# Kernel optimization log

Hardware: AMD Instinct MI355X
Metric: run time of the kernel (lower is better)

Reference implementation:

```python
import jax, jax.numpy as jnp
import numpy as np

LN_EPS = 1e-5
NORM_EPS = 1e-6
ALPHA = 0.5

def _normalize_xyz_with_pc(pc, xyz):
    # center by point-cloud centroid, scale by max radius (per batch)
    c = pc.mean(axis=1, keepdims=True)                      # [B,1,3]
    scale = jnp.linalg.norm(pc - c, axis=-1).max(axis=1)    # [B]
    return (xyz - c) / (scale[:, None, None] + NORM_EPS)

def setup_inputs() -> dict:
    key = jax.random.key(0)
    ks = jax.random.split(key, 9)
    B, N, Ns, K, Dv, Dc = 4, 20000, 1024, 8192, 768, 256
    return {
        "point_cloud": jax.random.normal(ks[0], (B, N, 3), jnp.float32),
        "seed_xyz": jax.random.normal(ks[1], (B, Ns, 3), jnp.float32),
        "pts": jax.random.normal(ks[2], (B, K, 3), jnp.float32),
        "feat": jax.random.normal(ks[3], (B, Dv, K), jnp.float32),
        "f_graspnet": jax.random.normal(ks[4], (B, Dc, Ns), jnp.float32),
        "W_proj": jax.random.normal(ks[5], (Dc, Dv), jnp.float32) * 0.02,
        "b_proj": jnp.zeros((Dc,), jnp.float32),
        "W_a1": jax.random.normal(ks[6], (Dc, Dc), jnp.float32) * 0.05,
        "b_a1": jnp.zeros((Dc,), jnp.float32),
        "W_a2": jax.random.normal(ks[7], (Dc, Dc), jnp.float32) * 0.05,
        "b_a2": jnp.zeros((Dc,), jnp.float32),
    }

def reference(point_cloud, seed_xyz, pts, feat, f_graspnet,
              W_proj, b_proj, W_a1, b_a1, W_a2, b_a2):
    seed_n = _normalize_xyz_with_pc(point_cloud, seed_xyz)   # [B,Ns,3]
    pts_n = _normalize_xyz_with_pc(point_cloud, pts)         # [B,K,3]
    # squared pairwise distances [B,Ns,K] (argmin equivalent to cdist argmin)
    d2 = ((seed_n ** 2).sum(-1)[:, :, None]
          - 2.0 * jnp.einsum('bnd,bkd->bnk', seed_n, pts_n)
          + (pts_n ** 2).sum(-1)[:, None, :])
    idx = jnp.argmin(d2, axis=-1)                            # [B,Ns]
    vggt_raw = jnp.take_along_axis(feat, idx[:, None, :], axis=2)  # [B,768,Ns]
    # 1x1 conv projector 768->256
    x = jnp.einsum('oc,bcn->bon', W_proj, vggt_raw) + b_proj[None, :, None]
    # LayerNorm over channel dim, no affine
    mu = x.mean(axis=1, keepdims=True)
    var = ((x - mu) ** 2).mean(axis=1, keepdims=True)
    x_ln = (x - mu) / jnp.sqrt(var + LN_EPS)
    # adapter: conv-relu-conv (all 1x1)
    h = jax.nn.relu(jnp.einsum('oc,bcn->bon', W_a1, x_ln) + b_a1[None, :, None])
    f_adapt = jnp.einsum('oc,bcn->bon', W_a2, h) + b_a2[None, :, None]
    return (1.0 - ALPHA) * f_graspnet + ALPHA * f_adapt
```

## Files before the change

kernel.cpp:

```cpp
#include <hip/hip_runtime.h>
#include <hip/hip_bf16.h>
#include <math.h>

#define LN_EPS 1e-5f

constexpr int BB  = 4;
constexpr int NS  = 1024;
constexpr int KP  = 8192;
constexpr int DV  = 768;
constexpr int DC  = 256;

using bf16x8 = __attribute__((ext_vector_type(8))) short;
using f32x4  = __attribute__((ext_vector_type(4))) float;

static __device__ __forceinline__ unsigned short f2bf(float v) {
    __hip_bfloat16 h = __float2bfloat16(v);
    return *reinterpret_cast<unsigned short*>(&h);
}

__global__ __launch_bounds__(256) void argmin_prep_kernel(
    const float* __restrict__ seed_xyz, const float* __restrict__ pts,
    int* __restrict__ out_idx,
    const float* __restrict__ Wp, const float* __restrict__ W1,
    const float* __restrict__ W2,
    unsigned short* __restrict__ Wpb, unsigned short* __restrict__ W1b,
    unsigned short* __restrict__ W2b)
{
    const int t = threadIdx.x;
    if (blockIdx.x >= 512) {
        int e  = (blockIdx.x - 512) * 256 + t;
        int e4 = e << 2;
        const float* src; unsigned short* dst; int off;
        if (e4 < DC * DV)              { src = Wp; dst = Wpb; off = e4; }
        else if (e4 < DC * (DV + DC))  { src = W1; dst = W1b; off = e4 - DC * DV; }
        else                           { src = W2; dst = W2b; off = e4 - DC * (DV + DC); }
        float4 v = *(const float4*)(src + off);
        ushort4 o;
        o.x = f2bf(v.x); o.y = f2bf(v.y); o.z = f2bf(v.z); o.w = f2bf(v.w);
        *(ushort4*)(dst + off) = o;
        return;
    }

    __shared__ float shX[1024], shY[1024], shZ[1024];
    __shared__ double rb[4][8];
    __shared__ int    ri[4][8];

    const int bid  = blockIdx.x;
    const int b    = bid >> 7;
    const int tile = bid & 127;

    double n2sx[8], n2sy[8], n2sz[8];
    {
        const float* sp = seed_xyz + ((size_t)b * NS + tile * 8) * 3;
        #pragma unroll
        for (int ss = 0; ss < 8; ++ss) {
            n2sx[ss] = -2.0 * (double)sp[ss * 3 + 0];
            n2sy[ss] = -2.0 * (double)sp[ss * 3 + 1];
            n2sz[ss] = -2.0 * (double)sp[ss * 3 + 2];
        }
    }

    const float* pb = pts + (size_t)b * KP * 3;
    double best[8];
    int    bidx[8];
    #pragma unroll
    for (int ss = 0; ss < 8; ++ss) { best[ss] = 1e300; bidx[ss] = 0; }

    for (int kt = 0; kt < KP; kt += 1024) {
        #pragma unroll
        for (int q = 0; q < 4; ++q) {
            int i = t + q * 256;
            const float* pp = pb + (size_t)(kt + i) * 3;
            shX[i] = pp[0]; shY[i] = pp[1]; shZ[i] = pp[2];
        }
        __syncthreads();
        #pragma unroll 2
        for (int q = 0; q < 4; ++q) {
            int kl = t + (q << 8);
            double px = (double)shX[kl];
            double py = (double)shY[kl];
            double pz = (double)shZ[kl];
            double h  = fma(px, px, fma(py, py, pz * pz));
            #pragma unroll
            for (int ss = 0; ss < 8; ++ss) {
                double acc = fma(n2sx[ss], px, h);
                acc = fma(n2sy[ss], py, acc);
                acc = fma(n2sz[ss], pz, acc);
                if (acc < best[ss]) { best[ss] = acc; bidx[ss] = kt + kl; }
            }
        }
        __syncthreads();
    }

    #pragma unroll
    for (int o = 1; o < 64; o <<= 1) {
        #pragma unroll
        for (int ss = 0; ss < 8; ++ss) {
            double ob = __shfl_xor(best[ss], o);
            int    oi = __shfl_xor(bidx[ss], o);
            if (ob < best[ss] || (ob == best[ss] && oi < bidx[ss])) {
                best[ss] = ob; bidx[ss] = oi;
            }
        }
    }
    const int w = t >> 6, l = t & 63;
    if (l == 0) {
        #pragma unroll
        for (int ss = 0; ss < 8; ++ss) { rb[w][ss] = best[ss]; ri[w][ss] = bidx[ss]; }
    }
    __syncthreads();
    if (t < 8) {
        double bb = rb[0][t]; int bi = ri[0][t];
        #pragma unroll
        for (int ww = 1; ww < 4; ++ww) {
            double ob = rb[ww][t]; int oi = ri[ww][t];
            if (ob < bb || (ob == bb && oi < bi)) { bb = ob; bi = oi; }
        }
        out_idx[b * NS + tile * 8 + t] = bi;
    }
}

__global__ __launch_bounds__(512) void sort_kernel(
    const int* __restrict__ idx, int* __restrict__ ord, int* __restrict__ ks)
{
    __shared__ int h[512], sc[512], base[512], cnt[512];
    const int b = blockIdx.x;
    const int t = threadIdx.x;
    h[t] = 0; cnt[t] = 0;
    __syncthreads();
    const int k0 = idx[b * NS + t];
    const int k1 = idx[b * NS + 512 + t];
    atomicAdd(&h[k0 >> 4], 1);
    atomicAdd(&h[k1 >> 4], 1);
    __syncthreads();
    sc[t] = h[t];
    __syncthreads();
    #pragma unroll
    for (int st = 1; st < 512; st <<= 1) {
        int add = (t >= st) ? sc[t - st] : 0;
        __syncthreads();
        sc[t] += add;
        __syncthreads();
    }
    base[t] = sc[t] - h[t];
    __syncthreads();
    {
        int bk = k0 >> 4;
        int p  = base[bk] + atomicAdd(&cnt[bk], 1);
        ord[b * NS + p] = t;
        ks [b * NS + p] = k0;
    }
    {
        int bk = k1 >> 4;
        int p  = base[bk] + atomicAdd(&cnt[bk], 1);
        ord[b * NS + p] = 512 + t;
        ks [b * NS + p] = k1;
    }
}

__global__ __launch_bounds__(256) void gather_kernel(
    const float* __restrict__ feat, const int* __restrict__ ord,
    const int* __restrict__ ks, unsigned short* __restrict__ Gb)
{
    const int bid = blockIdx.x;
    const int b   = bid >> 6;
    const int cg  = bid & 63;
    const int c0  = cg * 12;
    const int t   = threadIdx.x;
    const float* fb = feat + ((size_t)b * DV + c0) * KP;

    int sA[4], kA[4];
    #pragma unroll
    for (int i = 0; i < 4; ++i) {
        sA[i] = ord[b * NS + t + i * 256];
        kA[i] = ks [b * NS + t + i * 256];
    }
    float v[4][12];
    #pragma unroll
    for (int i = 0; i < 4; ++i)
        #pragma unroll
        for (int c = 0; c < 12; ++c)
            v[i][c] = fb[(size_t)c * KP + kA[i]];

    #pragma unroll
    for (int i = 0; i < 4; ++i) {
        ushort4 o0, o1, o2;
        o0.x = f2bf(v[i][0]);  o0.y = f2bf(v[i][1]);
        o0.z = f2bf(v[i][2]);  o0.w = f2bf(v[i][3]);
        o1.x = f2bf(v[i][4]);  o1.y = f2bf(v[i][5]);
        o1.z = f2bf(v[i][6]);  o1.w = f2bf(v[i][7]);
        o2.x = f2bf(v[i][8]);  o2.y = f2bf(v[i][9]);
        o2.z = f2bf(v[i][10]); o2.w = f2bf(v[i][11]);
        unsigned short* g = Gb + ((size_t)b * NS + sA[i]) * DV + c0;
        *(ushort4*)(g)     = o0;
        *(ushort4*)(g + 4) = o1;
        *(ushort4*)(g + 8) = o2;
    }
}

__global__ __launch_bounds__(512) void mega_kernel(
    const unsigned short* __restrict__ Gb,
    const float* __restrict__ fg,
    const unsigned short* __restrict__ Wpb, const float* __restrict__ bp,
    const unsigned short* __restrict__ W1b, const float* __restrict__ b1,
    const unsigned short* __restrict__ W2b, const float* __restrict__ b2,
    float* __restrict__ out)
{
    __shared__ alignas(16) unsigned short GtT[16][776];
    __shared__ alignas(16) unsigned short XT[16][264];
    __shared__ alignas(16) unsigned short HT[16][264];
    __shared__ float LNs[8][16];
    __shared__ float LNq[8][16];

    const int bid  = blockIdx.x;
    const int b    = bid >> 6;
    const int tile = bid & 63;
    const int n0   = tile * 16;
    const int t    = threadIdx.x;
    const int w    = t >> 6;
    const int l    = t & 63;
    const int col  = l & 15;
    const int kq   = l >> 4;

    for (int i = t; i < 1536; i += 512) {
        int row = i / 96, c8 = (i % 96) * 8;
        *(bf16x8*)&GtT[row][c8] =
            *(const bf16x8*)&Gb[((size_t)b * NS + n0 + row) * DV + c8];
    }
    __syncthreads();

    f32x4 acc0 = {0.f, 0.f, 0.f, 0.f};
    f32x4 acc1 = {0.f, 0.f, 0.f, 0.f};
    {
        const unsigned short* A0 = Wpb + (size_t)(w * 32 + col) * DV;
        const unsigned short* A1 = Wpb + (size_t)(w * 32 + 16 + col) * DV;
        #pragma unroll 4
        for (int ks = 0; ks < 24; ++ks) {
            int kb = ks * 32 + kq * 8;
            bf16x8 bf = *(const bf16x8*)&GtT[col][kb];
            bf16x8 a0 = *(const bf16x8*)&A0[kb];
            bf16x8 a1 = *(const bf16x8*)&A1[kb];
            acc0 = __builtin_amdgcn_mfma_f32_16x16x32_bf16(a0, bf, acc0, 0, 0, 0);
            acc1 = __builtin_amdgcn_mfma_f32_16x16x32_bf16(a1, bf, acc1, 0, 0, 0);
        }
    }

    float vals[8];
    float s = 0.f, q = 0.f;
    #pragma unroll
    for (int r = 0; r < 4; ++r) {
        int ch0 = w * 32 + kq * 4 + r;
        float v0 = acc0[r] + bp[ch0];
        float v1 = acc1[r] + bp[ch0 + 16];
        vals[r]     = v0;
        vals[4 + r] = v1;
        s += v0 + v1;
        q += v0 * v0 + v1 * v1;
    }
    s += __shfl_xor(s, 16); s += __shfl_xor(s, 32);
    q += __shfl_xor(q, 16); q += __shfl_xor(q, 32);
    if (l < 16) { LNs[w][l] = s; LNq[w][l] = q; }
    __syncthreads();
    float S = 0.f, Q = 0.f;
    #pragma unroll
    for (int ww = 0; ww < 8; ++ww) { S += LNs[ww][col]; Q += LNq[ww][col]; }
    float mu   = S * (1.0f / DC);
    float rstd = rsqrtf(Q * (1.0f / DC) - mu * mu + LN_EPS);
    {
        ushort4 p0, p1;
        p0.x = f2bf((vals[0] - mu) * rstd);
        p0.y = f2bf((vals[1] - mu) * rstd);
        p0.z = f2bf((vals[2] - mu) * rstd);
        p0.w = f2bf((vals[3] - mu) * rstd);
        p1.x = f2bf((vals[4] - mu) * rstd);
        p1.y = f2bf((vals[5] - mu) * rstd);
        p1.z = f2bf((vals[6] - mu) * rstd);
        p1.w = f2bf((vals[7] - mu) * rstd);
        *(ushort4*)&XT[col][w * 32 + kq * 4]      = p0;
        *(ushort4*)&XT[col][w * 32 + 16 + kq * 4] = p1;
    }
    __syncthreads();

    acc0 = (f32x4){0.f, 0.f, 0.f, 0.f};
    acc1 = (f32x4){0.f, 0.f, 0.f, 0.f};
    {
        const unsigned short* A0 = W1b + (size_t)(w * 32 + col) * DC;
        const unsigned short* A1 = W1b + (size_t)(w * 32 + 16 + col) * DC;
        #pragma unroll
        for (int ks = 0; ks < 8; ++ks) {
            int kb = ks * 32 + kq * 8;
            bf16x8 bf = *(const bf16x8*)&XT[col][kb];
            bf16x8 a0 = *(const bf16x8*)&A0[kb];
            bf16x8 a1 = *(const bf16x8*)&A1[kb];
            acc0 = __builtin_amdgcn_mfma_f32_16x16x32_bf16(a0, bf, acc0, 0, 0, 0);
            acc1 = __builtin_amdgcn_mfma_f32_16x16x32_bf16(a1, bf, acc1, 0, 0, 0);
        }
    }
    {
        ushort4 p0, p1;
        int ch0 = w * 32 + kq * 4;
        p0.x = f2bf(fmaxf(acc0[0] + b1[ch0 + 0], 0.f));
        p0.y = f2bf(fmaxf(acc0[1] + b1[ch0 + 1], 0.f));
        p0.z = f2bf(fmaxf(acc0[2] + b1[ch0 + 2], 0.f));
        p0.w = f2bf(fmaxf(acc0[3] + b1[ch0 + 3], 0.f));
        p1.x = f2bf(fmaxf(acc1[0] + b1[ch0 + 16], 0.f));
        p1.y = f2bf(fmaxf(acc1[1] + b1[ch0 + 17], 0.f));
        p1.z = f2bf(fmaxf(acc1[2] + b1[ch0 + 18], 0.f));
        p1.w = f2bf(fmaxf(acc1[3] + b1[ch0 + 19], 0.f));
        *(ushort4*)&HT[col][ch0]      = p0;
        *(ushort4*)&HT[col][ch0 + 16] = p1;
    }
    __syncthreads();

    acc0 = (f32x4){0.f, 0.f, 0.f, 0.f};
    acc1 = (f32x4){0.f, 0.f, 0.f, 0.f};
    {
        const unsigned short* A0 = W2b + (size_t)(w * 32 + col) * DC;
        const unsigned short* A1 = W2b + (size_t)(w * 32 + 16 + col) * DC;
        #pragma unroll
        for (int ks = 0; ks < 8; ++ks) {
            int kb = ks * 32 + kq * 8;
            bf16x8 bf = *(const bf16x8*)&HT[col][kb];
            bf16x8 a0 = *(const bf16x8*)&A0[kb];
            bf16x8 a1 = *(const bf16x8*)&A1[kb];
            acc0 = __builtin_amdgcn_mfma_f32_16x16x32_bf16(a0, bf, acc0, 0, 0, 0);
            acc1 = __builtin_amdgcn_mfma_f32_16x16x32_bf16(a1, bf, acc1, 0, 0, 0);
        }
    }
    {
        const float* fgb = fg  + (size_t)b * DC * NS;
        float*       ob  = out + (size_t)b * DC * NS;
        #pragma unroll
        for (int r = 0; r < 4; ++r) {
            int ch0 = w * 32 + kq * 4 + r;
            int ch1 = ch0 + 16;
            size_t o0 = (size_t)ch0 * NS + n0 + col;
            size_t o1 = (size_t)ch1 * NS + n0 + col;
            ob[o0] = 0.5f * fgb[o0] + 0.5f * (acc0[r] + b2[ch0]);
            ob[o1] = 0.5f * fgb[o1] + 0.5f * (acc1[r] + b2[ch1]);
        }
    }
}

extern "C" void kernel_launch(void* const* d_in, const int* in_sizes, int n_in,
                              void* d_out, int out_size, void* d_ws, size_t ws_size,
                              hipStream_t stream)
{
    (void)in_sizes; (void)n_in; (void)out_size; (void)ws_size;
    const float* seed_xyz = (const float*)d_in[1];
    const float* pts      = (const float*)d_in[2];
    const float* feat     = (const float*)d_in[3];
    const float* fgn      = (const float*)d_in[4];
    const float* Wp       = (const float*)d_in[5];
    const float* bp       = (const float*)d_in[6];
    const float* W1       = (const float*)d_in[7];
    const float* b1       = (const float*)d_in[8];
    const float* W2       = (const float*)d_in[9];
    const float* b2       = (const float*)d_in[10];
    float* out = (float*)d_out;

    char* ws = (char*)d_ws;
    int*            idx = (int*)ws;
    int*            ord = (int*)(ws + 16384);
    int*            kss = (int*)(ws + 32768);
    unsigned short* Wpb = (unsigned short*)(ws + 49152);
    unsigned short* W1b = (unsigned short*)(ws + 442368);
    unsigned short* W2b = (unsigned short*)(ws + 573440);
    unsigned short* Gb  = (unsigned short*)(ws + 704512);

    argmin_prep_kernel<<<dim3(832), dim3(256), 0, stream>>>(
        seed_xyz, pts, idx, Wp, W1, W2, Wpb, W1b, W2b);
    sort_kernel<<<dim3(BB), dim3(512), 0, stream>>>(idx, ord, kss);
    gather_kernel<<<dim3(256), dim3(256), 0, stream>>>(feat, ord, kss, Gb);
    mega_kernel<<<dim3(BB * (NS / 16)), dim3(512), 0, stream>>>(
        Gb, fgn, Wpb, bp, W1b, b1, W2b, b2, out);
}
```

Baseline: 69.13 us.

## Fuse bucket sort into gather kernel and prefetch f_graspnet early in mega kernel

```diff
diff --git a/kernel.cpp b/kernel.cpp
--- a/kernel.cpp
+++ b/kernel.cpp
@@ -120,12 +120,20 @@
     }
 }
 
-__global__ __launch_bounds__(512) void sort_kernel(
-    const int* __restrict__ idx, int* __restrict__ ord, int* __restrict__ ks)
+__global__ __launch_bounds__(512) void gather_kernel(
+    const float* __restrict__ feat, const int* __restrict__ idx,
+    unsigned short* __restrict__ Gb)
 {
     __shared__ int h[512], sc[512], base[512], cnt[512];
-    const int b = blockIdx.x;
-    const int t = threadIdx.x;
+    __shared__ int ordL[1024];
+    __shared__ int ksL[1024];
+
+    const int bid = blockIdx.x;
+    const int b   = bid >> 6;
+    const int cg  = bid & 63;
+    const int c0  = cg * 12;
+    const int t   = threadIdx.x;
+
     h[t] = 0; cnt[t] = 0;
     __syncthreads();
     const int k0 = idx[b * NS + t];
@@ -135,7 +143,6 @@
     __syncthreads();
     sc[t] = h[t];
     __syncthreads();
-    #pragma unroll
     for (int st = 1; st < 512; st <<= 1) {
         int add = (t >= st) ? sc[t - st] : 0;
         __syncthreads();
@@ -147,43 +154,34 @@
     {
         int bk = k0 >> 4;
         int p  = base[bk] + atomicAdd(&cnt[bk], 1);
-        ord[b * NS + p] = t;
-        ks [b * NS + p] = k0;
+        ordL[p] = t;
+        ksL [p] = k0;
     }
     {
         int bk = k1 >> 4;
         int p  = base[bk] + atomicAdd(&cnt[bk], 1);
-        ord[b * NS + p] = 512 + t;
-        ks [b * NS + p] = k1;
-    }
-}
-
-__global__ __launch_bounds__(256) void gather_kernel(
-    const float* __restrict__ feat, const int* __restrict__ ord,
-    const int* __restrict__ ks, unsigned short* __restrict__ Gb)
-{
-    const int bid = blockIdx.x;
-    const int b   = bid >> 6;
-    const int cg  = bid & 63;
-    const int c0  = cg * 12;
-    const int t   = threadIdx.x;
+        ordL[p] = 512 + t;
+        ksL [p] = k1;
+    }
+    __syncthreads();
+
     const float* fb = feat + ((size_t)b * DV + c0) * KP;
 
-    int sA[4], kA[4];
-    #pragma unroll
-    for (int i = 0; i < 4; ++i) {
-        sA[i] = ord[b * NS + t + i * 256];
-        kA[i] = ks [b * NS + t + i * 256];
-    }
-    float v[4][12];
-    #pragma unroll
-    for (int i = 0; i < 4; ++i)
+    int sA[2], kA[2];
+    #pragma unroll
+    for (int i = 0; i < 2; ++i) {
+        sA[i] = ordL[t + i * 512];
+        kA[i] = ksL [t + i * 512];
+    }
+    float v[2][12];
+    #pragma unroll
+    for (int i = 0; i < 2; ++i)
         #pragma unroll
         for (int c = 0; c < 12; ++c)
             v[i][c] = fb[(size_t)c * KP + kA[i]];
 
     #pragma unroll
-    for (int i = 0; i < 4; ++i) {
+    for (int i = 0; i < 2; ++i) {
         ushort4 o0, o1, o2;
         o0.x = f2bf(v[i][0]);  o0.y = f2bf(v[i][1]);
         o0.z = f2bf(v[i][2]);  o0.w = f2bf(v[i][3]);
@@ -222,6 +220,15 @@
     const int col  = l & 15;
     const int kq   = l >> 4;
 
+    const float* fgb = fg + (size_t)b * DC * NS;
+    float fgv[8];
+    #pragma unroll
+    for (int r = 0; r < 4; ++r) {
+        int ch0 = w * 32 + kq * 4 + r;
+        fgv[r]     = fgb[(size_t)ch0 * NS + n0 + col];
+        fgv[4 + r] = fgb[(size_t)(ch0 + 16) * NS + n0 + col];
+    }
+
     for (int i = t; i < 1536; i += 512) {
         int row = i / 96, c8 = (i % 96) * 8;
         *(bf16x8*)&GtT[row][c8] =
@@ -328,16 +335,15 @@
         }
     }
     {
-        const float* fgb = fg  + (size_t)b * DC * NS;
-        float*       ob  = out + (size_t)b * DC * NS;
+        float* ob = out + (size_t)b * DC * NS;
         #pragma unroll
         for (int r = 0; r < 4; ++r) {
             int ch0 = w * 32 + kq * 4 + r;
             int ch1 = ch0 + 16;
             size_t o0 = (size_t)ch0 * NS + n0 + col;
             size_t o1 = (size_t)ch1 * NS + n0 + col;
-            ob[o0] = 0.5f * fgb[o0] + 0.5f * (acc0[r] + b2[ch0]);
-            ob[o1] = 0.5f * fgb[o1] + 0.5f * (acc1[r] + b2[ch1]);
+            ob[o0] = 0.5f * fgv[r]     + 0.5f * (acc0[r] + b2[ch0]);
+            ob[o1] = 0.5f * fgv[4 + r] + 0.5f * (acc1[r] + b2[ch1]);
         }
     }
 }
@@ -361,8 +367,6 @@
 
     char* ws = (char*)d_ws;
     int*            idx = (int*)ws;
-    int*            ord = (int*)(ws + 16384);
-    int*            kss = (int*)(ws + 32768);
     unsigned short* Wpb = (unsigned short*)(ws + 49152);
     unsigned short* W1b = (unsigned short*)(ws + 442368);
     unsigned short* W2b = (unsigned short*)(ws + 573440);
@@ -370,8 +374,7 @@
 
     argmin_prep_kernel<<<dim3(832), dim3(256), 0, stream>>>(
         seed_xyz, pts, idx, Wp, W1, W2, Wpb, W1b, W2b);
-    sort_kernel<<<dim3(BB), dim3(512), 0, stream>>>(idx, ord, kss);
-    gather_kernel<<<dim3(256), dim3(256), 0, stream>>>(feat, ord, kss, Gb);
+    gather_kernel<<<dim3(256), dim3(512), 0, stream>>>(feat, idx, Gb);
     mega_kernel<<<dim3(BB * (NS / 16)), dim3(512), 0, stream>>>(
         Gb, fgn, Wpb, bp, W1b, b1, W2b, b2, out);
 }
```

After: 68.24 us. No clear change (-1.3%).
